# Kernel optimization log

Hardware: AMD Instinct MI355X
Metric: run time of the kernel (lower is better)

## Reference

```python
import jax, jax.numpy as jnp
import numpy as np

EPS_DEN = 1e-6
EPS_LN = 1e-6


def setup_inputs() -> dict:
    key = jax.random.key(0)
    ks = jax.random.split(key, 10)
    B, H, NH = 64, 2048, 8
    HD = H // NH
    q = jax.random.normal(ks[0], (B, 1, H), jnp.float32)
    k = jax.random.normal(ks[1], (B, 1, H), jnp.float32)
    v = jax.random.normal(ks[2], (B, 1, H), jnp.float32)
    c = jax.random.normal(ks[3], (B, NH, HD, HD), jnp.float32)
    n = jax.random.normal(ks[4], (B, NH, HD, 1), jnp.float32)
    m = jnp.zeros((B, NH, 1, 1), jnp.float32)
    wi_kernel = 0.01 * jax.random.normal(ks[5], (3 * H, NH), jnp.float32)
    wi_bias = 0.1 * jax.random.normal(ks[6], (NH,), jnp.float32)
    wf_kernel = 0.01 * jax.random.normal(ks[7], (3 * H, NH), jnp.float32)
    wf_bias = jnp.linspace(3.0, 6.0, NH, dtype=jnp.float32)  # linspace_init(3,6)
    ln_scale = jnp.ones((NH, HD), jnp.float32)
    return {"q": q, "k": k, "v": v, "c": c, "n": n, "m": m,
            "wi_kernel": wi_kernel, "wi_bias": wi_bias,
            "wf_kernel": wf_kernel, "wf_bias": wf_bias, "ln_scale": ln_scale}


def reference(q, k, v, c, n, m, wi_kernel, wi_bias, wf_kernel, wf_bias, ln_scale):
    B, S, H = q.shape            # S == 1 (single-step cell)
    NH, HD = ln_scale.shape
    qkv = jnp.concatenate([q, k, v], axis=-1)           # (B,1,3H)
    qh = q.reshape(B, NH, HD, S)                        # (B,NH,HD,1)
    kh = k.reshape(B, NH, HD, S) / jnp.sqrt(jnp.asarray(HD, q.dtype))
    vh = v.reshape(B, NH, HD, S)
    # gates: Dense(3H -> NH), then (B,1,NH) -> (B,NH,1,1)
    i_tilde = (qkv @ wi_kernel + wi_bias).swapaxes(-1, -2)[..., None]
    f_tilde = (qkv @ wf_kernel + wf_bias).swapaxes(-1, -2)[..., None]
    log_f = -jax.nn.softplus(-f_tilde)                  # log sigmoid(f_tilde)
    m_new = jnp.maximum(log_f + m, i_tilde)             # log-domain stabilizer
    i_prime = jnp.exp(i_tilde - m_new)
    f_prime = jnp.exp(log_f + m - m_new)
    c_new = f_prime * c + i_prime * (kh @ vh.swapaxes(-1, -2))   # (B,NH,HD,HD)
    n_new = f_prime * n + i_prime * kh                            # (B,NH,HD,1)
    nominator = qh.swapaxes(-1, -2) @ c_new                       # (B,NH,1,HD)
    denominator = jnp.maximum(jnp.abs(qh.swapaxes(-1, -2) @ n_new), jnp.exp(-m_new))
    h_tilde = nominator / (denominator + EPS_DEN)                 # (B,NH,1,HD)
    # MultiHeadLayerNorm: normalize over head_dim, per-head scale, no bias
    mu = h_tilde.mean(-1, keepdims=True)
    var = h_tilde.var(-1, keepdims=True)
    h_norm = (h_tilde - mu) * jax.lax.rsqrt(var + EPS_LN) * ln_scale[None, :, None, :]
    h_norm = h_norm.swapaxes(1, 2).reshape(B, S, -1)              # (B,1,H)
    return (c_new, n_new, m_new, h_norm)
```

## Files before the change

### kernel.cpp

```cpp
#include <hip/hip_runtime.h>
#include <math.h>

constexpr int Bb  = 64;
constexpr int Hh  = 2048;
constexpr int NHh = 8;
constexpr int HDd = 256;

constexpr size_t C_OFF = 0;
constexpr size_t N_OFF = (size_t)Bb * NHh * HDd * HDd;
constexpr size_t M_OFF = N_OFF + (size_t)Bb * NHh * HDd;
constexpr size_t H_OFF = M_OFF + (size_t)Bb * NHh;

__global__ __launch_bounds__(256) void gates_kernel(
    const float* __restrict__ q, const float* __restrict__ k,
    const float* __restrict__ v, const float* __restrict__ m_in,
    const float* __restrict__ wi_k, const float* __restrict__ wi_b,
    const float* __restrict__ wf_k, const float* __restrict__ wf_b,
    float* __restrict__ ws, float* __restrict__ out_m)
{
    const int b    = blockIdx.x;
    const int t    = threadIdx.x;
    const int lane = t & 63;
    const int wv   = t >> 6;

    float ai[8], af[8];
#pragma unroll
    for (int i = 0; i < 8; ++i) { ai[i] = 0.f; af[i] = 0.f; }

#pragma unroll 4
    for (int j = 0; j < 24; ++j) {
        const int r = t + 256 * j;
        float x;
        if (r < Hh)            x = q[b * Hh + r];
        else if (r < 2 * Hh)   x = k[b * Hh + r - Hh];
        else                   x = v[b * Hh + r - 2 * Hh];

        const float4 wa = *(const float4*)(wi_k + (size_t)r * 8);
        const float4 wb = *(const float4*)(wi_k + (size_t)r * 8 + 4);
        ai[0] = fmaf(x, wa.x, ai[0]); ai[1] = fmaf(x, wa.y, ai[1]);
        ai[2] = fmaf(x, wa.z, ai[2]); ai[3] = fmaf(x, wa.w, ai[3]);
        ai[4] = fmaf(x, wb.x, ai[4]); ai[5] = fmaf(x, wb.y, ai[5]);
        ai[6] = fmaf(x, wb.z, ai[6]); ai[7] = fmaf(x, wb.w, ai[7]);

        const float4 fa = *(const float4*)(wf_k + (size_t)r * 8);
        const float4 fb = *(const float4*)(wf_k + (size_t)r * 8 + 4);
        af[0] = fmaf(x, fa.x, af[0]); af[1] = fmaf(x, fa.y, af[1]);
        af[2] = fmaf(x, fa.z, af[2]); af[3] = fmaf(x, fa.w, af[3]);
        af[4] = fmaf(x, fb.x, af[4]); af[5] = fmaf(x, fb.y, af[5]);
        af[6] = fmaf(x, fb.z, af[6]); af[7] = fmaf(x, fb.w, af[7]);
    }

#pragma unroll
    for (int i = 0; i < 8; ++i) {
#pragma unroll
        for (int o = 32; o > 0; o >>= 1) {
            ai[i] += __shfl_down(ai[i], o, 64);
            af[i] += __shfl_down(af[i], o, 64);
        }
    }

    __shared__ float s_part[4][16];
    if (lane == 0) {
#pragma unroll
        for (int i = 0; i < 8; ++i) {
            s_part[wv][i]     = ai[i];
            s_part[wv][8 + i] = af[i];
        }
    }
    __syncthreads();

    if (t < 8) {
        const int h = t;
        const float it = s_part[0][h] + s_part[1][h] + s_part[2][h] + s_part[3][h]
                         + wi_b[h];
        const float ft = s_part[0][8 + h] + s_part[1][8 + h] + s_part[2][8 + h]
                         + s_part[3][8 + h] + wf_b[h];
        const float logf_ = -(fmaxf(-ft, 0.f) + log1pf(expf(-fabsf(ft))));
        const float m_old = m_in[b * NHh + h];
        const float m_new = fmaxf(logf_ + m_old, it);
        const float ip    = expf(it - m_new);
        const float fp    = expf(logf_ + m_old - m_new);
        const int blk = b * NHh + h;
        ws[blk * 4 + 0] = fp;
        ws[blk * 4 + 1] = ip;
        ws[blk * 4 + 2] = m_new;
        out_m[blk] = m_new;
    }
}

__global__ __launch_bounds__(256) void cell_kernel(
    const float* __restrict__ q, const float* __restrict__ k,
    const float* __restrict__ v, const float* __restrict__ c_in,
    const float* __restrict__ n_in, const float* __restrict__ ln_s,
    const float* __restrict__ ws, float* __restrict__ out)
{
    const int blk  = blockIdx.x;
    const int b    = blk >> 3;
    const int h    = blk & 7;
    const int t    = threadIdx.x;
    const int lane = t & 63;
    const int wv   = t >> 6;

    __shared__ float  s_q[HDd];
    __shared__ float  s_k[HDd];
    __shared__ float  s_v[HDd];
    __shared__ float4 s_nom[4][64];
    __shared__ float  s_dred[4];

    const float fp = ws[blk * 4 + 0];
    const float ip = ws[blk * 4 + 1];
    const float mn = ws[blk * 4 + 2];

    const float qv = q[b * Hh + h * HDd + t];
    const float kv = k[b * Hh + h * HDd + t] * 0.0625f;
    s_q[t] = qv;
    s_k[t] = kv;
    s_v[t] = v[b * Hh + h * HDd + t];

    const float nn = fmaf(fp, n_in[(size_t)blk * HDd + t], ip * kv);
    out[N_OFF + (size_t)blk * HDd + t] = nn;
    float pd = qv * nn;
#pragma unroll
    for (int o = 32; o > 0; o >>= 1) pd += __shfl_down(pd, o, 64);
    if (lane == 0) s_dred[wv] = pd;

    __syncthreads();

    const size_t cbase = (size_t)blk * (HDd * HDd);
    const float4* cin  = (const float4*)(c_in + cbase);
    float4*       cout = (float4*)(out + C_OFF + cbase);
    const float4  vh4  = ((const float4*)s_v)[lane];
    float4 nom = make_float4(0.f, 0.f, 0.f, 0.f);

#pragma unroll 8
    for (int d1 = wv; d1 < HDd; d1 += 4) {
        const float a   = ip * s_k[d1];
        const float qh1 = s_q[d1];
        const int   idx = d1 * 64 + lane;
        const float4 cv = cin[idx];
        float4 cn;
        cn.x = fmaf(fp, cv.x, a * vh4.x);
        cn.y = fmaf(fp, cv.y, a * vh4.y);
        cn.z = fmaf(fp, cv.z, a * vh4.z);
        cn.w = fmaf(fp, cv.w, a * vh4.w);
        cout[idx] = cn;
        nom.x = fmaf(qh1, cn.x, nom.x);
        nom.y = fmaf(qh1, cn.y, nom.y);
        nom.z = fmaf(qh1, cn.z, nom.z);
        nom.w = fmaf(qh1, cn.w, nom.w);
    }
    s_nom[wv][lane] = nom;
    __syncthreads();

    if (t < 64) {
        float4 n0 = s_nom[0][t], n1 = s_nom[1][t], n2 = s_nom[2][t], n3 = s_nom[3][t];
        float4 nt;
        nt.x = n0.x + n1.x + n2.x + n3.x;
        nt.y = n0.y + n1.y + n2.y + n3.y;
        nt.z = n0.z + n1.z + n2.z + n3.z;
        nt.w = n0.w + n1.w + n2.w + n3.w;

        const float dd    = s_dred[0] + s_dred[1] + s_dred[2] + s_dred[3];
        const float denom = fmaxf(fabsf(dd), expf(-mn)) + 1e-6f;

        float4 ht;
        ht.x = nt.x / denom; ht.y = nt.y / denom;
        ht.z = nt.z / denom; ht.w = nt.w / denom;

        float s = ht.x + ht.y + ht.z + ht.w;
#pragma unroll
        for (int o = 32; o > 0; o >>= 1) s += __shfl_down(s, o, 64);
        s = __shfl(s, 0, 64);
        const float mu = s * (1.f / 256.f);

        float vs = (ht.x - mu) * (ht.x - mu) + (ht.y - mu) * (ht.y - mu)
                 + (ht.z - mu) * (ht.z - mu) + (ht.w - mu) * (ht.w - mu);
#pragma unroll
        for (int o = 32; o > 0; o >>= 1) vs += __shfl_down(vs, o, 64);
        vs = __shfl(vs, 0, 64);
        const float rs = rsqrtf(vs * (1.f / 256.f) + 1e-6f);

        const float4 lns = ((const float4*)(ln_s + h * HDd))[t];
        float4 hn;
        hn.x = (ht.x - mu) * rs * lns.x;
        hn.y = (ht.y - mu) * rs * lns.y;
        hn.z = (ht.z - mu) * rs * lns.z;
        hn.w = (ht.w - mu) * rs * lns.w;
        ((float4*)(out + H_OFF + (size_t)b * Hh + h * HDd))[t] = hn;
    }
}

extern "C" void kernel_launch(void* const* d_in, const int* in_sizes, int n_in,
                              void* d_out, int out_size, void* d_ws, size_t ws_size,
                              hipStream_t stream)
{
    const float* q    = (const float*)d_in[0];
    const float* k    = (const float*)d_in[1];
    const float* v    = (const float*)d_in[2];
    const float* c    = (const float*)d_in[3];
    const float* n    = (const float*)d_in[4];
    const float* m    = (const float*)d_in[5];
    const float* wi_k = (const float*)d_in[6];
    const float* wi_b = (const float*)d_in[7];
    const float* wf_k = (const float*)d_in[8];
    const float* wf_b = (const float*)d_in[9];
    const float* ln_s = (const float*)d_in[10];
    float* out = (float*)d_out;
    float* ws  = (float*)d_ws;

    gates_kernel<<<dim3(Bb), dim3(256), 0, stream>>>(
        q, k, v, m, wi_k, wi_b, wf_k, wf_b, ws, out + M_OFF);
    cell_kernel<<<dim3(Bb * NHh), dim3(256), 0, stream>>>(
        q, k, v, c, n, ln_s, ws, out);
}
```

Baseline: 271.7 us.

## Fuse gate computation into cell kernel and widen blocks to 1024 threads

Merges the separate gates kernel into the cell kernel, so each (batch, head) block computes its own gate dot product over the 3H input with 1024 threads. This removes one launch and the workspace round-trip. The cost is that each block re-reads the full q/k/v row and a strided column of the gate weights, so that gate work is done eight times per batch. Block size also rises from 256 to 1024 threads, giving the 256 KB c-update loop 16 waves per block to hide memory latency, with the partial numerators reduced through a larger shared buffer.

```diff
diff --git a/kernel.cpp b/kernel.cpp
--- a/kernel.cpp
+++ b/kernel.cpp
@@ -11,88 +11,13 @@
 constexpr size_t M_OFF = N_OFF + (size_t)Bb * NHh * HDd;
 constexpr size_t H_OFF = M_OFF + (size_t)Bb * NHh;
 
-__global__ __launch_bounds__(256) void gates_kernel(
+__global__ __launch_bounds__(1024, 8) void fused_cell_kernel(
     const float* __restrict__ q, const float* __restrict__ k,
-    const float* __restrict__ v, const float* __restrict__ m_in,
+    const float* __restrict__ v, const float* __restrict__ c_in,
+    const float* __restrict__ n_in, const float* __restrict__ m_in,
     const float* __restrict__ wi_k, const float* __restrict__ wi_b,
     const float* __restrict__ wf_k, const float* __restrict__ wf_b,
-    float* __restrict__ ws, float* __restrict__ out_m)
-{
-    const int b    = blockIdx.x;
-    const int t    = threadIdx.x;
-    const int lane = t & 63;
-    const int wv   = t >> 6;
-
-    float ai[8], af[8];
-#pragma unroll
-    for (int i = 0; i < 8; ++i) { ai[i] = 0.f; af[i] = 0.f; }
-
-#pragma unroll 4
-    for (int j = 0; j < 24; ++j) {
-        const int r = t + 256 * j;
-        float x;
-        if (r < Hh)            x = q[b * Hh + r];
-        else if (r < 2 * Hh)   x = k[b * Hh + r - Hh];
-        else                   x = v[b * Hh + r - 2 * Hh];
-
-        const float4 wa = *(const float4*)(wi_k + (size_t)r * 8);
-        const float4 wb = *(const float4*)(wi_k + (size_t)r * 8 + 4);
-        ai[0] = fmaf(x, wa.x, ai[0]); ai[1] = fmaf(x, wa.y, ai[1]);
-        ai[2] = fmaf(x, wa.z, ai[2]); ai[3] = fmaf(x, wa.w, ai[3]);
-        ai[4] = fmaf(x, wb.x, ai[4]); ai[5] = fmaf(x, wb.y, ai[5]);
-        ai[6] = fmaf(x, wb.z, ai[6]); ai[7] = fmaf(x, wb.w, ai[7]);
-
-        const float4 fa = *(const float4*)(wf_k + (size_t)r * 8);
-        const float4 fb = *(const float4*)(wf_k + (size_t)r * 8 + 4);
-        af[0] = fmaf(x, fa.x, af[0]); af[1] = fmaf(x, fa.y, af[1]);
-        af[2] = fmaf(x, fa.z, af[2]); af[3] = fmaf(x, fa.w, af[3]);
-        af[4] = fmaf(x, fb.x, af[4]); af[5] = fmaf(x, fb.y, af[5]);
-        af[6] = fmaf(x, fb.z, af[6]); af[7] = fmaf(x, fb.w, af[7]);
-    }
-
-#pragma unroll
-    for (int i = 0; i < 8; ++i) {
-#pragma unroll
-        for (int o = 32; o > 0; o >>= 1) {
-            ai[i] += __shfl_down(ai[i], o, 64);
-            af[i] += __shfl_down(af[i], o, 64);
-        }
-    }
-
-    __shared__ float s_part[4][16];
-    if (lane == 0) {
-#pragma unroll
-        for (int i = 0; i < 8; ++i) {
-            s_part[wv][i]     = ai[i];
-            s_part[wv][8 + i] = af[i];
-        }
-    }
-    __syncthreads();
-
-    if (t < 8) {
-        const int h = t;
-        const float it = s_part[0][h] + s_part[1][h] + s_part[2][h] + s_part[3][h]
-                         + wi_b[h];
-        const float ft = s_part[0][8 + h] + s_part[1][8 + h] + s_part[2][8 + h]
-                         + s_part[3][8 + h] + wf_b[h];
-        const float logf_ = -(fmaxf(-ft, 0.f) + log1pf(expf(-fabsf(ft))));
-        const float m_old = m_in[b * NHh + h];
-        const float m_new = fmaxf(logf_ + m_old, it);
-        const float ip    = expf(it - m_new);
-        const float fp    = expf(logf_ + m_old - m_new);
-        const int blk = b * NHh + h;
-        ws[blk * 4 + 0] = fp;
-        ws[blk * 4 + 1] = ip;
-        ws[blk * 4 + 2] = m_new;
-        out_m[blk] = m_new;
-    }
-}
-
-__global__ __launch_bounds__(256) void cell_kernel(
-    const float* __restrict__ q, const float* __restrict__ k,
-    const float* __restrict__ v, const float* __restrict__ c_in,
-    const float* __restrict__ n_in, const float* __restrict__ ln_s,
-    const float* __restrict__ ws, float* __restrict__ out)
+    const float* __restrict__ ln_s, float* __restrict__ out)
 {
     const int blk  = blockIdx.x;
     const int b    = blk >> 3;
@@ -104,27 +29,62 @@
     __shared__ float  s_q[HDd];
     __shared__ float  s_k[HDd];
     __shared__ float  s_v[HDd];
-    __shared__ float4 s_nom[4][64];
+    __shared__ float4 s_nom[16][64];
+    __shared__ float  s_red[16][2];
     __shared__ float  s_dred[4];
+    __shared__ float  s_gate[3];
 
-    const float fp = ws[blk * 4 + 0];
-    const float ip = ws[blk * 4 + 1];
-    const float mn = ws[blk * 4 + 2];
+    float ai = 0.f, af = 0.f;
+#pragma unroll
+    for (int j = 0; j < 6; ++j) {
+        const int r = t + 1024 * j;
+        float x;
+        if (r < Hh)            x = q[b * Hh + r];
+        else if (r < 2 * Hh)   x = k[b * Hh + r - Hh];
+        else                   x = v[b * Hh + r - 2 * Hh];
+        ai = fmaf(x, wi_k[(size_t)r * 8 + h], ai);
+        af = fmaf(x, wf_k[(size_t)r * 8 + h], af);
+    }
+#pragma unroll
+    for (int o = 32; o > 0; o >>= 1) {
+        ai += __shfl_down(ai, o, 64);
+        af += __shfl_down(af, o, 64);
+    }
+    if (lane == 0) { s_red[wv][0] = ai; s_red[wv][1] = af; }
 
-    const float qv = q[b * Hh + h * HDd + t];
-    const float kv = k[b * Hh + h * HDd + t] * 0.0625f;
-    s_q[t] = qv;
-    s_k[t] = kv;
-    s_v[t] = v[b * Hh + h * HDd + t];
+    if (t < HDd) {
+        s_q[t] = q[b * Hh + h * HDd + t];
+        s_k[t] = k[b * Hh + h * HDd + t] * 0.0625f;
+        s_v[t] = v[b * Hh + h * HDd + t];
+    }
+    __syncthreads();
 
-    const float nn = fmaf(fp, n_in[(size_t)blk * HDd + t], ip * kv);
-    out[N_OFF + (size_t)blk * HDd + t] = nn;
-    float pd = qv * nn;
+    if (t == 0) {
+        float it = wi_b[h], ft = wf_b[h];
 #pragma unroll
-    for (int o = 32; o > 0; o >>= 1) pd += __shfl_down(pd, o, 64);
-    if (lane == 0) s_dred[wv] = pd;
+        for (int w = 0; w < 16; ++w) { it += s_red[w][0]; ft += s_red[w][1]; }
+        const float logf_ = -(fmaxf(-ft, 0.f) + log1pf(expf(-fabsf(ft))));
+        const float m_old = m_in[blk];
+        const float m_new = fmaxf(logf_ + m_old, it);
+        s_gate[0] = expf(logf_ + m_old - m_new);
+        s_gate[1] = expf(it - m_new);
+        s_gate[2] = m_new;
+        out[M_OFF + blk] = m_new;
+    }
+    __syncthreads();
 
-    __syncthreads();
+    const float fp = s_gate[0];
+    const float ip = s_gate[1];
+    const float mn = s_gate[2];
+
+    if (t < HDd) {
+        const float nn = fmaf(fp, n_in[(size_t)blk * HDd + t], ip * s_k[t]);
+        out[N_OFF + (size_t)blk * HDd + t] = nn;
+        float pd = s_q[t] * nn;
+#pragma unroll
+        for (int o = 32; o > 0; o >>= 1) pd += __shfl_down(pd, o, 64);
+        if (lane == 0) s_dred[wv] = pd;
+    }
 
     const size_t cbase = (size_t)blk * (HDd * HDd);
     const float4* cin  = (const float4*)(c_in + cbase);
@@ -132,8 +92,9 @@
     const float4  vh4  = ((const float4*)s_v)[lane];
     float4 nom = make_float4(0.f, 0.f, 0.f, 0.f);
 
-#pragma unroll 8
-    for (int d1 = wv; d1 < HDd; d1 += 4) {
+#pragma unroll 4
+    for (int j = 0; j < 16; ++j) {
+        const int   d1  = 16 * j + wv;
         const float a   = ip * s_k[d1];
         const float qh1 = s_q[d1];
         const int   idx = d1 * 64 + lane;
@@ -153,19 +114,20 @@
     __syncthreads();
 
     if (t < 64) {
-        float4 n0 = s_nom[0][t], n1 = s_nom[1][t], n2 = s_nom[2][t], n3 = s_nom[3][t];
-        float4 nt;
-        nt.x = n0.x + n1.x + n2.x + n3.x;
-        nt.y = n0.y + n1.y + n2.y + n3.y;
-        nt.z = n0.z + n1.z + n2.z + n3.z;
-        nt.w = n0.w + n1.w + n2.w + n3.w;
+        float4 nt = make_float4(0.f, 0.f, 0.f, 0.f);
+#pragma unroll
+        for (int w = 0; w < 16; ++w) {
+            const float4 p = s_nom[w][t];
+            nt.x += p.x; nt.y += p.y; nt.z += p.z; nt.w += p.w;
+        }
 
         const float dd    = s_dred[0] + s_dred[1] + s_dred[2] + s_dred[3];
         const float denom = fmaxf(fabsf(dd), expf(-mn)) + 1e-6f;
+        const float rden  = 1.f / denom;
 
         float4 ht;
-        ht.x = nt.x / denom; ht.y = nt.y / denom;
-        ht.z = nt.z / denom; ht.w = nt.w / denom;
+        ht.x = nt.x * rden; ht.y = nt.y * rden;
+        ht.z = nt.z * rden; ht.w = nt.w * rden;
 
         float s = ht.x + ht.y + ht.z + ht.w;
 #pragma unroll
@@ -206,10 +168,7 @@
     const float* wf_b = (const float*)d_in[9];
     const float* ln_s = (const float*)d_in[10];
     float* out = (float*)d_out;
-    float* ws  = (float*)d_ws;
 
-    gates_kernel<<<dim3(Bb), dim3(256), 0, stream>>>(
-        q, k, v, m, wi_k, wi_b, wf_k, wf_b, ws, out + M_OFF);
-    cell_kernel<<<dim3(Bb * NHh), dim3(256), 0, stream>>>(
-        q, k, v, c, n, ln_s, ws, out);
+    fused_cell_kernel<<<dim3(Bb * NHh), dim3(1024), 0, stream>>>(
+        q, k, v, c, n, m, wi_k, wi_b, wf_k, wf_b, ln_s, out);
 }
```

Result: no change. 269.2 us (-0.9%).

## Split C-state streaming across 8 blocks per head with atomic nominator reduction

Applied to the files above, without the earlier changes.

Moves the n update and denominator computation into the gates kernel, splits each head's 256x256 C update across 8 blocks of 32 rows (4096 blocks instead of 512), and accumulates the nominator with atomicAdd into a zero-initialised output buffer. A separate small kernel then applies the denominator and layer norm. This targets under-occupancy of the memory-bound C stream and adds nontemporal loads and stores, at the cost of an extra launch and float atomics, which make the summation order nondeterministic.

```diff
diff --git a/kernel.cpp b/kernel.cpp
--- a/kernel.cpp
+++ b/kernel.cpp
@@ -1,5 +1,7 @@
 #include <hip/hip_runtime.h>
 #include <math.h>
+
+typedef float f32x4 __attribute__((ext_vector_type(4)));
 
 constexpr int Bb  = 64;
 constexpr int Hh  = 2048;
@@ -13,15 +15,22 @@
 
 __global__ __launch_bounds__(256) void gates_kernel(
     const float* __restrict__ q, const float* __restrict__ k,
-    const float* __restrict__ v, const float* __restrict__ m_in,
+    const float* __restrict__ v, const float* __restrict__ n_in,
+    const float* __restrict__ m_in,
     const float* __restrict__ wi_k, const float* __restrict__ wi_b,
     const float* __restrict__ wf_k, const float* __restrict__ wf_b,
-    float* __restrict__ ws, float* __restrict__ out_m)
+    float* __restrict__ ws, float* __restrict__ out)
 {
     const int b    = blockIdx.x;
     const int t    = threadIdx.x;
     const int lane = t & 63;
     const int wv   = t >> 6;
+
+    {
+        f32x4 z = {0.f, 0.f, 0.f, 0.f};
+        f32x4* zp = (f32x4*)(out + H_OFF + (size_t)b * Hh) + t * 2;
+        zp[0] = z; zp[1] = z;
+    }
 
     float ai[8], af[8];
 #pragma unroll
@@ -35,19 +44,19 @@
         else if (r < 2 * Hh)   x = k[b * Hh + r - Hh];
         else                   x = v[b * Hh + r - 2 * Hh];
 
-        const float4 wa = *(const float4*)(wi_k + (size_t)r * 8);
-        const float4 wb = *(const float4*)(wi_k + (size_t)r * 8 + 4);
-        ai[0] = fmaf(x, wa.x, ai[0]); ai[1] = fmaf(x, wa.y, ai[1]);
-        ai[2] = fmaf(x, wa.z, ai[2]); ai[3] = fmaf(x, wa.w, ai[3]);
-        ai[4] = fmaf(x, wb.x, ai[4]); ai[5] = fmaf(x, wb.y, ai[5]);
-        ai[6] = fmaf(x, wb.z, ai[6]); ai[7] = fmaf(x, wb.w, ai[7]);
-
-        const float4 fa = *(const float4*)(wf_k + (size_t)r * 8);
-        const float4 fb = *(const float4*)(wf_k + (size_t)r * 8 + 4);
-        af[0] = fmaf(x, fa.x, af[0]); af[1] = fmaf(x, fa.y, af[1]);
-        af[2] = fmaf(x, fa.z, af[2]); af[3] = fmaf(x, fa.w, af[3]);
-        af[4] = fmaf(x, fb.x, af[4]); af[5] = fmaf(x, fb.y, af[5]);
-        af[6] = fmaf(x, fb.z, af[6]); af[7] = fmaf(x, fb.w, af[7]);
+        const f32x4 wa = *(const f32x4*)(wi_k + (size_t)r * 8);
+        const f32x4 wb = *(const f32x4*)(wi_k + (size_t)r * 8 + 4);
+        ai[0] = fmaf(x, wa[0], ai[0]); ai[1] = fmaf(x, wa[1], ai[1]);
+        ai[2] = fmaf(x, wa[2], ai[2]); ai[3] = fmaf(x, wa[3], ai[3]);
+        ai[4] = fmaf(x, wb[0], ai[4]); ai[5] = fmaf(x, wb[1], ai[5]);
+        ai[6] = fmaf(x, wb[2], ai[6]); ai[7] = fmaf(x, wb[3], ai[7]);
+
+        const f32x4 fa = *(const f32x4*)(wf_k + (size_t)r * 8);
+        const f32x4 fb = *(const f32x4*)(wf_k + (size_t)r * 8 + 4);
+        af[0] = fmaf(x, fa[0], af[0]); af[1] = fmaf(x, fa[1], af[1]);
+        af[2] = fmaf(x, fa[2], af[2]); af[3] = fmaf(x, fa[3], af[3]);
+        af[4] = fmaf(x, fb[0], af[4]); af[5] = fmaf(x, fb[1], af[5]);
+        af[6] = fmaf(x, fb[2], af[6]); af[7] = fmaf(x, fb[3], af[7]);
     }
 
 #pragma unroll
@@ -60,6 +69,7 @@
     }
 
     __shared__ float s_part[4][16];
+    __shared__ float s_g[8][3];
     if (lane == 0) {
 #pragma unroll
         for (int i = 0; i < 8; ++i) {
@@ -78,116 +88,129 @@
         const float logf_ = -(fmaxf(-ft, 0.f) + log1pf(expf(-fabsf(ft))));
         const float m_old = m_in[b * NHh + h];
         const float m_new = fmaxf(logf_ + m_old, it);
+        const float fp    = expf(logf_ + m_old - m_new);
         const float ip    = expf(it - m_new);
-        const float fp    = expf(logf_ + m_old - m_new);
         const int blk = b * NHh + h;
+        s_g[h][0] = fp; s_g[h][1] = ip; s_g[h][2] = m_new;
         ws[blk * 4 + 0] = fp;
         ws[blk * 4 + 1] = ip;
         ws[blk * 4 + 2] = m_new;
-        out_m[blk] = m_new;
-    }
-}
-
-__global__ __launch_bounds__(256) void cell_kernel(
+        out[M_OFF + blk] = m_new;
+    }
+    __syncthreads();
+
+    float pd[8];
+#pragma unroll
+    for (int h = 0; h < 8; ++h) {
+        const float kv = k[b * Hh + h * HDd + t] * 0.0625f;
+        const float nn = fmaf(s_g[h][0], n_in[((size_t)b * 8 + h) * HDd + t],
+                              s_g[h][1] * kv);
+        out[N_OFF + ((size_t)b * 8 + h) * HDd + t] = nn;
+        pd[h] = q[b * Hh + h * HDd + t] * nn;
+    }
+#pragma unroll
+    for (int h = 0; h < 8; ++h)
+#pragma unroll
+        for (int o = 32; o > 0; o >>= 1) pd[h] += __shfl_down(pd[h], o, 64);
+
+    __shared__ float s_dp[4][8];
+    if (lane == 0) {
+#pragma unroll
+        for (int h = 0; h < 8; ++h) s_dp[wv][h] = pd[h];
+    }
+    __syncthreads();
+    if (t < 8) {
+        const float dd = s_dp[0][t] + s_dp[1][t] + s_dp[2][t] + s_dp[3][t];
+        ws[(b * 8 + t) * 4 + 3] = fmaxf(fabsf(dd), expf(-s_g[t][2])) + 1e-6f;
+    }
+}
+
+__global__ __launch_bounds__(256) void stream_kernel(
     const float* __restrict__ q, const float* __restrict__ k,
     const float* __restrict__ v, const float* __restrict__ c_in,
-    const float* __restrict__ n_in, const float* __restrict__ ln_s,
     const float* __restrict__ ws, float* __restrict__ out)
 {
     const int blk  = blockIdx.x;
-    const int b    = blk >> 3;
-    const int h    = blk & 7;
+    const int tile = blk >> 3;
+    const int s    = blk & 7;
+    const int b    = tile >> 3;
+    const int h    = tile & 7;
     const int t    = threadIdx.x;
     const int lane = t & 63;
     const int wv   = t >> 6;
 
-    __shared__ float  s_q[HDd];
-    __shared__ float  s_k[HDd];
-    __shared__ float  s_v[HDd];
-    __shared__ float4 s_nom[4][64];
-    __shared__ float  s_dred[4];
-
-    const float fp = ws[blk * 4 + 0];
-    const float ip = ws[blk * 4 + 1];
-    const float mn = ws[blk * 4 + 2];
-
-    const float qv = q[b * Hh + h * HDd + t];
-    const float kv = k[b * Hh + h * HDd + t] * 0.0625f;
-    s_q[t] = qv;
-    s_k[t] = kv;
-    s_v[t] = v[b * Hh + h * HDd + t];
-
-    const float nn = fmaf(fp, n_in[(size_t)blk * HDd + t], ip * kv);
-    out[N_OFF + (size_t)blk * HDd + t] = nn;
-    float pd = qv * nn;
-#pragma unroll
-    for (int o = 32; o > 0; o >>= 1) pd += __shfl_down(pd, o, 64);
-    if (lane == 0) s_dred[wv] = pd;
-
-    __syncthreads();
-
-    const size_t cbase = (size_t)blk * (HDd * HDd);
-    const float4* cin  = (const float4*)(c_in + cbase);
-    float4*       cout = (float4*)(out + C_OFF + cbase);
-    const float4  vh4  = ((const float4*)s_v)[lane];
-    float4 nom = make_float4(0.f, 0.f, 0.f, 0.f);
-
-#pragma unroll 8
-    for (int d1 = wv; d1 < HDd; d1 += 4) {
-        const float a   = ip * s_k[d1];
-        const float qh1 = s_q[d1];
-        const int   idx = d1 * 64 + lane;
-        const float4 cv = cin[idx];
-        float4 cn;
-        cn.x = fmaf(fp, cv.x, a * vh4.x);
-        cn.y = fmaf(fp, cv.y, a * vh4.y);
-        cn.z = fmaf(fp, cv.z, a * vh4.z);
-        cn.w = fmaf(fp, cv.w, a * vh4.w);
-        cout[idx] = cn;
-        nom.x = fmaf(qh1, cn.x, nom.x);
-        nom.y = fmaf(qh1, cn.y, nom.y);
-        nom.z = fmaf(qh1, cn.z, nom.z);
-        nom.w = fmaf(qh1, cn.w, nom.w);
+    __shared__ float s_kh[32];
+    __shared__ float s_qh[32];
+    __shared__ f32x4 s_nom[4][64];
+
+    if (t < 32) {
+        const int r = s * 32 + t;
+        s_kh[t] = k[b * Hh + h * HDd + r] * 0.0625f;
+        s_qh[t] = q[b * Hh + h * HDd + r];
+    }
+    const float fp  = ws[tile * 4 + 0];
+    const float ip  = ws[tile * 4 + 1];
+    const f32x4 vh4 = ((const f32x4*)(v + b * Hh + h * HDd))[lane];
+    __syncthreads();
+
+    const size_t cbase = (size_t)tile * (HDd * HDd);
+    const f32x4* cin   = (const f32x4*)(c_in + cbase);
+    f32x4*       cout  = (f32x4*)(out + C_OFF + cbase);
+    f32x4 nom = {0.f, 0.f, 0.f, 0.f};
+    const int rb = wv * 8;
+
+#pragma unroll
+    for (int j = 0; j < 8; ++j) {
+        const int   r   = rb + j;
+        const float a   = ip * s_kh[r];
+        const float qh1 = s_qh[r];
+        const int   idx = (s * 32 + r) * 64 + lane;
+        f32x4 cv = __builtin_nontemporal_load(cin + idx);
+        f32x4 cn = fp * cv + a * vh4;
+        __builtin_nontemporal_store(cn, cout + idx);
+        nom += qh1 * cn;
     }
     s_nom[wv][lane] = nom;
     __syncthreads();
 
     if (t < 64) {
-        float4 n0 = s_nom[0][t], n1 = s_nom[1][t], n2 = s_nom[2][t], n3 = s_nom[3][t];
-        float4 nt;
-        nt.x = n0.x + n1.x + n2.x + n3.x;
-        nt.y = n0.y + n1.y + n2.y + n3.y;
-        nt.z = n0.z + n1.z + n2.z + n3.z;
-        nt.w = n0.w + n1.w + n2.w + n3.w;
-
-        const float dd    = s_dred[0] + s_dred[1] + s_dred[2] + s_dred[3];
-        const float denom = fmaxf(fabsf(dd), expf(-mn)) + 1e-6f;
-
-        float4 ht;
-        ht.x = nt.x / denom; ht.y = nt.y / denom;
-        ht.z = nt.z / denom; ht.w = nt.w / denom;
-
-        float s = ht.x + ht.y + ht.z + ht.w;
-#pragma unroll
-        for (int o = 32; o > 0; o >>= 1) s += __shfl_down(s, o, 64);
-        s = __shfl(s, 0, 64);
-        const float mu = s * (1.f / 256.f);
-
-        float vs = (ht.x - mu) * (ht.x - mu) + (ht.y - mu) * (ht.y - mu)
-                 + (ht.z - mu) * (ht.z - mu) + (ht.w - mu) * (ht.w - mu);
-#pragma unroll
-        for (int o = 32; o > 0; o >>= 1) vs += __shfl_down(vs, o, 64);
-        vs = __shfl(vs, 0, 64);
-        const float rs = rsqrtf(vs * (1.f / 256.f) + 1e-6f);
-
-        const float4 lns = ((const float4*)(ln_s + h * HDd))[t];
-        float4 hn;
-        hn.x = (ht.x - mu) * rs * lns.x;
-        hn.y = (ht.y - mu) * rs * lns.y;
-        hn.z = (ht.z - mu) * rs * lns.z;
-        hn.w = (ht.w - mu) * rs * lns.w;
-        ((float4*)(out + H_OFF + (size_t)b * Hh + h * HDd))[t] = hn;
-    }
+        f32x4 sum = s_nom[0][t] + s_nom[1][t] + s_nom[2][t] + s_nom[3][t];
+        float* dst = out + H_OFF + (size_t)tile * HDd + t * 4;
+        atomicAdd(dst + 0, sum[0]);
+        atomicAdd(dst + 1, sum[1]);
+        atomicAdd(dst + 2, sum[2]);
+        atomicAdd(dst + 3, sum[3]);
+    }
+}
+
+__global__ __launch_bounds__(64) void ln_kernel(
+    const float* __restrict__ ln_s, const float* __restrict__ ws,
+    float* __restrict__ out)
+{
+    const int blk  = blockIdx.x;
+    const int h    = blk & 7;
+    const int lane = threadIdx.x;
+
+    float* hp = out + H_OFF + (size_t)blk * HDd;
+    const f32x4 nt   = ((const f32x4*)hp)[lane];
+    const float rden = 1.f / ws[blk * 4 + 3];
+    f32x4 ht = nt * rden;
+
+    float s = ht[0] + ht[1] + ht[2] + ht[3];
+#pragma unroll
+    for (int o = 32; o > 0; o >>= 1) s += __shfl_down(s, o, 64);
+    s = __shfl(s, 0, 64);
+    const float mu = s * (1.f / 256.f);
+
+    const f32x4 d = ht - mu;
+    float vs = d[0] * d[0] + d[1] * d[1] + d[2] * d[2] + d[3] * d[3];
+#pragma unroll
+    for (int o = 32; o > 0; o >>= 1) vs += __shfl_down(vs, o, 64);
+    vs = __shfl(vs, 0, 64);
+    const float rs = rsqrtf(vs * (1.f / 256.f) + 1e-6f);
+
+    const f32x4 lns = ((const f32x4*)(ln_s + h * HDd))[lane];
+    ((f32x4*)hp)[lane] = d * rs * lns;
 }
 
 extern "C" void kernel_launch(void* const* d_in, const int* in_sizes, int n_in,
@@ -209,7 +232,8 @@
     float* ws  = (float*)d_ws;
 
     gates_kernel<<<dim3(Bb), dim3(256), 0, stream>>>(
-        q, k, v, m, wi_k, wi_b, wf_k, wf_b, ws, out + M_OFF);
-    cell_kernel<<<dim3(Bb * NHh), dim3(256), 0, stream>>>(
-        q, k, v, c, n, ln_s, ws, out);
-}
+        q, k, v, n, m, wi_k, wi_b, wf_k, wf_b, ws, out);
+    stream_kernel<<<dim3(Bb * NHh * 8), dim3(256), 0, stream>>>(
+        q, k, v, c, ws, out);
+    ln_kernel<<<dim3(Bb * NHh), dim3(64), 0, stream>>>(ln_s, ws, out);
+}
```

After: 262.3 us (median of 2 runs). 1.04x faster.
